# Performance work log

Measured on AMD Instinct MI355X. Metric: run time of the kernel, lower is better.

## Reference

```python
import jax, jax.numpy as jnp
import numpy as np

B, T, C = 16, 2048, 512
G = 2                 # groups
V = 320               # num_vars
D = C // G            # var_dim = 256
GAMMA = 0.25
GN_EPS = 1e-5


def setup_inputs() -> dict:
    key = jax.random.key(0)
    k1, k2, k3 = jax.random.split(key, 3)
    x = jax.random.normal(k1, (B, T, C), dtype=jnp.float32)
    # grouped 1x1 conv weight: (out_channels, in_channels_per_group) = (C, D)
    conv_w = jax.random.normal(k2, (C, D), dtype=jnp.float32) * (1.0 / np.sqrt(D))
    gn_w = jnp.ones((C,), dtype=jnp.float32)
    gn_b = jnp.zeros((C,), dtype=jnp.float32)
    embedding = 0.01 * jax.random.normal(k3, (V, G, D), dtype=jnp.float32)
    return {"x": x, "conv_w": conv_w, "gn_w": gn_w, "gn_b": gn_b, "embedding": embedding}


def reference(x, conv_w, gn_w, gn_b, embedding):
    # x: [B, T, C] (time_first=True) -> [B, C, T]
    xt = jnp.transpose(x, (0, 2, 1))
    # grouped 1x1 conv == per-group matmul
    xg = xt.reshape(B, G, D, T)                      # [B, G, D_in, T]
    wg = conv_w.reshape(G, D, D)                     # [G, D_out, D_in]
    h = jnp.einsum('bgit,goi->bgot', xg, wg)         # [B, G, D, T]
    # Fp32GroupNorm over (D, T) per (B, G)
    mu = h.mean(axis=(2, 3), keepdims=True)
    var = ((h - mu) ** 2).mean(axis=(2, 3), keepdims=True)
    hn = (h - mu) * jax.lax.rsqrt(var + GN_EPS)
    ze = hn.reshape(B, C, T) * gn_w[None, :, None] + gn_b[None, :, None]  # [B, C, T]

    ze_ = ze.reshape(B, G, D, T).transpose(0, 3, 1, 2)  # [B, T, G, D]
    # squared distances to codebook (same argmin as L2 norm)
    e_sq = (embedding ** 2).sum(-1).T                    # [G, V]
    d2 = ((ze_ ** 2).sum(-1)[..., None]
          - 2.0 * jnp.einsum('btgd,vgd->btgv', ze_, embedding)
          + e_sq[None, None])                            # [B, T, G, V]
    idx = jnp.argmin(d2, axis=-1)                        # [B, T, G] int32

    zq = embedding[idx, jnp.arange(G)[None, None, :]]    # [B, T, G, D]
    zq = zq.reshape(B, T, C).transpose(0, 2, 1)          # [B, C, T]

    # straight-through
    x_st = jax.lax.stop_gradient(zq) + (ze - jax.lax.stop_gradient(ze))
    x_out = jnp.transpose(x_st, (0, 2, 1))               # back to [B, T, C]

    # code perplexity from one-hot usage counts
    flat_idx = idx.reshape(-1, G)                        # [B*T, G]
    counts = jnp.zeros((V, G), dtype=jnp.float32).at[flat_idx, jnp.arange(G)[None, :]].add(1.0)
    hard_probs = counts.T / jnp.float32(B * T)           # [G, V]
    code_perplexity = jnp.exp(-jnp.sum(hard_probs * jnp.log(hard_probs + 1e-7), axis=-1)).sum()

    latent_loss = jnp.mean((zq - jax.lax.stop_gradient(ze)) ** 2)
    commitment_loss = jnp.mean((ze - jax.lax.stop_gradient(zq)) ** 2)
    kmeans_loss = latent_loss + GAMMA * commitment_loss
    return x_out, kmeans_loss, code_perplexity
```

## Files before the change

kernel.cpp:

```cpp
#include <hip/hip_runtime.h>
#include <math.h>

#define BB 16
#define TT 2048
#define CC 512
#define GG 2
#define DD 256
#define VV 320
#define DT (DD*TT)
#define NOUT ((size_t)BB*TT*CC)

#define OFF_H      0ULL
#define SZ_H       ((size_t)BB*GG*TT*DD*4)
#define OFF_PART   (OFF_H + SZ_H)
#define OFF_MUSIG  (OFF_PART + 4096ULL*2*8)
#define OFF_ESQ    (OFF_MUSIG + 32ULL*2*4)
#define OFF_CNT    (OFF_ESQ + (size_t)GG*VV*4)
#define OFF_LOSS   (OFF_CNT + (size_t)GG*VV*4)
#define OFF_EMBH   67180032ULL
#define OFF_WH     (OFF_EMBH + 327680ULL)
#define OFF_WL     (OFF_WH + 262144ULL)

typedef _Float16 half8   __attribute__((ext_vector_type(8)));
typedef _Float16 half4_t __attribute__((ext_vector_type(4)));
typedef float    f32x4   __attribute__((ext_vector_type(4)));

#define MARGIN 2e-3f
#define CAP 16

#define GLOAD_LDS16(g, l) \
  __builtin_amdgcn_global_load_lds((const __attribute__((address_space(1))) void*)(g), \
                                   (__attribute__((address_space(3))) void*)(l), 16, 0, 0)

__global__ __launch_bounds__(256) void k_emb(const float* __restrict__ emb,
                                             const float* __restrict__ w,
                                             _Float16* __restrict__ embHp,
                                             _Float16* __restrict__ wHp,
                                             _Float16* __restrict__ wLp,
                                             float* __restrict__ esq,
                                             unsigned* __restrict__ counts,
                                             float* __restrict__ loss) {
  int blk = blockIdx.x;
  int tid = threadIdx.x;
  if (blk == 40) {
    for (int i = tid; i < GG*VV; i += 256) counts[i] = 0u;
    if (tid == 0) *loss = 0.0f;
    return;
  }
  if (blk >= 41) {
    int wblk = blk - 41;
    int g = wblk >> 3, c = wblk & 7;
    int o = tid;
    const float* wrow = w + (size_t)(g*DD + o)*DD + (c << 5);
    #pragma unroll
    for (int hgrp = 0; hgrp < 4; ++hgrp) {
      float4 f1 = *(const float4*)(wrow + (hgrp << 2));
      float4 f2 = *(const float4*)(wrow + (hgrp << 2) + 16);
      float fv[8] = {f1.x, f1.y, f1.z, f1.w, f2.x, f2.y, f2.z, f2.w};
      half8 vh, vl;
      #pragma unroll
      for (int e = 0; e < 8; ++e) {
        _Float16 hh = (_Float16)fv[e];
        vh[e] = hh;
        vl[e] = (_Float16)(fv[e] - (float)hh);
      }
      size_t base = (((((size_t)(g*8 + c)) << 2) + hgrp) << 8) + o;
      *(half8*)(wHp + (base << 3)) = vh;
      *(half8*)(wLp + (base << 3)) = vl;
    }
    return;
  }
  int g = blk / 20;
  int v0 = (blk % 20) * 16;
  int vl = tid >> 4, dl = tid & 15;
  int v = v0 + vl;
  double sq = 0.0;
  #pragma unroll
  for (int k = 0; k < 16; k++) {
    int d = dl + (k << 4);
    float e = emb[((size_t)v*GG + g)*DD + d];
    sq += (double)e * (double)e;
  }
  #pragma unroll
  for (int m = 1; m < 16; m <<= 1) sq += __shfl_xor(sq, m);
  if (dl == 0) esq[g*VV + v] = (float)sq;

  const int hgrp = dl >> 2, jb = dl & 3;
  #pragma unroll
  for (int c = 0; c < 8; ++c) {
    int k0 = (c << 5) + (hgrp << 2) + jb;
    int k1 = k0 + 16;
    float e0 = emb[((size_t)v*GG + g)*DD + k0];
    float e1 = emb[((size_t)v*GG + g)*DD + k1];
    size_t base = (((size_t)(g*8 + c)*4 + hgrp)*320 + v)*8;
    embHp[base + jb]     = (_Float16)e0;
    embHp[base + jb + 4] = (_Float16)e1;
  }
}

__global__ __launch_bounds__(256, 2) void k_conv2(const float* __restrict__ x,
                                                  const _Float16* __restrict__ wH,
                                                  const _Float16* __restrict__ wL,
                                                  float* __restrict__ h,
                                                  double* __restrict__ part) {
  __shared__ __align__(16) char BsC[65536];
  __shared__ double r1[4], r2[4];
  const int bid = blockIdx.x;
  const int bg = bid >> 4, tt = bid & 15;
  const int b = bg >> 1, g = bg & 1;
  const int tid = threadIdx.x;
  const int wv = tid >> 6, lane = tid & 63;
  const int l15 = tid & 15, lh = lane >> 4;
  const int t0w = (tt << 7) + (wv << 5);

  f32x4 acc[2][16];
  #pragma unroll
  for (int tf = 0; tf < 2; ++tf)
    #pragma unroll
    for (int vf = 0; vf < 16; ++vf) acc[tf][vf] = 0.0f;

  const char* WHg = (const char*)(wH + ((size_t)g << 16));
  const char* WLg = (const char*)(wL + ((size_t)g << 16));
  const float* xb0 = x + ((size_t)(b*TT + t0w + l15)*CC + g*DD + (lh << 2));
  const float* xb1 = xb0 + ((size_t)16)*CC;

  {
    const char* sH = WHg + wv*4096 + lane*16;
    const char* sL = WLg + wv*4096 + lane*16;
    char* dH = BsC + wv*4096;
    char* dL = BsC + 32768 + wv*4096;
    #pragma unroll
    for (int i = 0; i < 4; ++i) {
      GLOAD_LDS16(sH + i*1024, dH + i*1024);
      GLOAD_LDS16(sL + i*1024, dL + i*1024);
    }
  }
  float4 p00 = *(const float4*)(xb0);
  float4 p01 = *(const float4*)(xb0 + 16);
  float4 p10 = *(const float4*)(xb1);
  float4 p11 = *(const float4*)(xb1 + 16);
  __syncthreads();

  int cur = 0;
  #pragma unroll 1
  for (int c = 0; c < 8; ++c) {
    if (c < 7) {
      const char* sH = WHg + (size_t)(c + 1)*16384 + wv*4096 + lane*16;
      const char* sL = WLg + (size_t)(c + 1)*16384 + wv*4096 + lane*16;
      char* dH = BsC + (cur ^ 1)*16384 + wv*4096;
      char* dL = BsC + 32768 + (cur ^ 1)*16384 + wv*4096;
      #pragma unroll
      for (int i = 0; i < 4; ++i) {
        GLOAD_LDS16(sH + i*1024, dH + i*1024);
        GLOAD_LDS16(sL + i*1024, dL + i*1024);
      }
    }
    float4 c00 = p00, c01 = p01, c10 = p10, c11 = p11;
    if (c < 7) {
      const int off = (c + 1) << 5;
      p00 = *(const float4*)(xb0 + off);
      p01 = *(const float4*)(xb0 + off + 16);
      p10 = *(const float4*)(xb1 + off);
      p11 = *(const float4*)(xb1 + off + 16);
    }
    half8 ah[2], al[2];
    {
      float fv0[8] = {c00.x, c00.y, c00.z, c00.w, c01.x, c01.y, c01.z, c01.w};
      float fv1[8] = {c10.x, c10.y, c10.z, c10.w, c11.x, c11.y, c11.z, c11.w};
      #pragma unroll
      for (int e = 0; e < 8; ++e) {
        _Float16 h0 = (_Float16)fv0[e];
        ah[0][e] = h0; al[0][e] = (_Float16)(fv0[e] - (float)h0);
        _Float16 h1 = (_Float16)fv1[e];
        ah[1][e] = h1; al[1][e] = (_Float16)(fv1[e] - (float)h1);
      }
    }
    const char* BH = BsC + cur*16384;
    const char* BL = BsC + 32768 + cur*16384;
    #pragma unroll
    for (int vf = 0; vf < 16; ++vf) {
      const int o = (vf << 4) + l15;
      const int bo = ((lh << 8) + o) << 4;
      half8 bh = *(const half8*)(BH + bo);
      half8 bl = *(const half8*)(BL + bo);
      #pragma unroll
      for (int tf = 0; tf < 2; ++tf) {
        acc[tf][vf] = __builtin_amdgcn_mfma_f32_16x16x32_f16(ah[tf], bh, acc[tf][vf], 0, 0, 0);
        acc[tf][vf] = __builtin_amdgcn_mfma_f32_16x16x32_f16(al[tf], bh, acc[tf][vf], 0, 0, 0);
        acc[tf][vf] = __builtin_amdgcn_mfma_f32_16x16x32_f16(ah[tf], bl, acc[tf][vf], 0, 0, 0);
      }
    }
    __syncthreads();
    cur ^= 1;
  }

  double s1 = 0.0, s2 = 0.0;
  {
    float* hb = h + (size_t)bg*TT*DD;
    #pragma unroll
    for (int tf = 0; tf < 2; ++tf) {
      #pragma unroll
      for (int reg = 0; reg < 4; ++reg) {
        const int t = t0w + (tf << 4) + (lh << 2) + reg;
        float* hrow = hb + (size_t)t*DD + l15;
        #pragma unroll
        for (int vf = 0; vf < 16; ++vf) {
          float v = acc[tf][vf][reg];
          hrow[vf << 4] = v;
          double dv = (double)v;
          s1 += dv; s2 += dv*dv;
        }
      }
    }
  }
  #pragma unroll
  for (int m = 32; m > 0; m >>= 1) { s1 += __shfl_down(s1, m); s2 += __shfl_down(s2, m); }
  if (lane == 0) { r1[wv] = s1; r2[wv] = s2; }
  __syncthreads();
  if (tid == 0) {
    part[(size_t)bid*2]     = r1[0] + r1[1] + r1[2] + r1[3];
    part[(size_t)bid*2 + 1] = r2[0] + r2[1] + r2[2] + r2[3];
  }
}

__global__ void k_stats(const double* __restrict__ part, float* __restrict__ musig) {
  int i = threadIdx.x;
  if (i < BB*GG) {
    double s1 = 0.0, s2 = 0.0;
    for (int r = 0; r < 16; r++) { s1 += part[(i*16 + r)*2]; s2 += part[(i*16 + r)*2 + 1]; }
    double mu  = s1 / (double)DT;
    double var = s2 / (double)DT - mu*mu;
    double rs  = 1.0 / sqrt(var + 1e-5);
    musig[i*2]     = (float)mu;
    musig[i*2 + 1] = (float)rs;
  }
}

__global__ __launch_bounds__(256, 2) void k_vq2(const float* __restrict__ h,
                                                const float* __restrict__ musig,
                                                const float* __restrict__ gn_w,
                                                const float* __restrict__ gn_b,
                                                const _Float16* __restrict__ embH,
                                                const float* __restrict__ esq,
                                                const float* __restrict__ emb,
                                                float* __restrict__ out,
                                                unsigned* __restrict__ counts,
                                                float* __restrict__ loss) {
  __shared__ __align__(16) char smem[43008];
  float*  esqs    = (float*)smem;
  int*    candcnt = (int*)(smem + 1280);
  int*    bestv   = (int*)(smem + 1792);
  int*    slowl   = (int*)(smem + 2304);
  int*    nslow   = (int*)(smem + 2816);
  unsigned short* cand = (unsigned short*)(smem + 2832);
  float*  redf    = (float*)(smem + 6944);
  float*  gnws    = (float*)(smem + 40960);
  float*  gnbs    = (float*)(smem + 41984);

  const int bid = blockIdx.x;
  const int bg  = bid >> 4;
  const int t0  = (bid & 15) << 7;
  const int b = bg >> 1, g = bg & 1;
  const int tid = threadIdx.x;
  const int lane = tid & 63, wv = tid >> 6;
  const int l15 = tid & 15, lh = lane >> 4;
  const float mu = musig[bg*2], rs = musig[bg*2 + 1];
  const float* hb = h + ((size_t)bg*TT + t0)*DD;

  gnws[tid] = gn_w[g*DD + tid];
  gnbs[tid] = gn_b[g*DD + tid];

  f32x4 acc[2][20];
  #pragma unroll
  for (int tf = 0; tf < 2; ++tf)
    #pragma unroll
    for (int vf = 0; vf < 20; ++vf) acc[tf][vf] = 0.0f;

  const char* gBH = (const char*)(embH + (size_t)(g*8)*10240);
  const float* gwp = gn_w + g*DD;
  const float* gbp = gn_b + g*DD;

  const float* hb0 = hb + (size_t)((wv << 5) + l15)*DD + (lh << 2);
  const float* hb1 = hb0 + ((size_t)16)*DD;

  {
    const char* sB = gBH + wv*5120 + lane*16;
    char* dB = smem + wv*5120;
    #pragma unroll
    for (int i = 0; i < 5; ++i) GLOAD_LDS16(sB + i*1024, dB + i*1024);
  }
  float4 p00 = *(const float4*)(hb0);
  float4 p01 = *(const float4*)(hb0 + 16);
  float4 p10 = *(const float4*)(hb1);
  float4 p11 = *(const float4*)(hb1 + 16);
  __syncthreads();

  int cur = 0;
  #pragma unroll 1
  for (int c = 0; c < 8; ++c) {
    if (c < 7) {
      const char* sB = gBH + (size_t)(c + 1)*20480 + wv*5120 + lane*16;
      char* dB = smem + (cur ^ 1)*20480 + wv*5120;
      #pragma unroll
      for (int i = 0; i < 5; ++i) GLOAD_LDS16(sB + i*1024, dB + i*1024);
    }
    float4 c00 = p00, c01 = p01, c10 = p10, c11 = p11;
    if (c < 7) {
      const int off = (c + 1) << 5;
      p00 = *(const float4*)(hb0 + off);
      p01 = *(const float4*)(hb0 + off + 16);
      p10 = *(const float4*)(hb1 + off);
      p11 = *(const float4*)(hb1 + off + 16);
    }
    const int c32 = c << 5;
    half8 ah[2];
    {
      float4 w1 = *(const float4*)(gwp + c32 + (lh << 2));
      float4 w2 = *(const float4*)(gwp + c32 + (lh << 2) + 16);
      float4 b1 = *(const float4*)(gbp + c32 + (lh << 2));
      float4 b2 = *(const float4*)(gbp + c32 + (lh << 2) + 16);
      float wv_[8] = {w1.x, w1.y, w1.z, w1.w, w2.x, w2.y, w2.z, w2.w};
      float bv_[8] = {b1.x, b1.y, b1.z, b1.w, b2.x, b2.y, b2.z, b2.w};
      float fv0[8] = {c00.x, c00.y, c00.z, c00.w, c01.x, c01.y, c01.z, c01.w};
      float fv1[8] = {c10.x, c10.y, c10.z, c10.w, c11.x, c11.y, c11.z, c11.w};
      #pragma unroll
      for (int e = 0; e < 8; ++e) {
        float z0 = __fmul_rn(__fsub_rn(fv0[e], mu), rs);
        z0 = __fadd_rn(__fmul_rn(z0, wv_[e]), bv_[e]);
        ah[0][e] = (_Float16)z0;
        float z1 = __fmul_rn(__fsub_rn(fv1[e], mu), rs);
        z1 = __fadd_rn(__fmul_rn(z1, wv_[e]), bv_[e]);
        ah[1][e] = (_Float16)z1;
      }
    }
    const char* BH = smem + cur*20480;
    #pragma unroll
    for (int vf = 0; vf < 20; ++vf) {
      const int v = (vf << 4) + l15;
      half8 bh = *(const half8*)(BH + ((lh*320 + v) << 4));
      #pragma unroll
      for (int tf = 0; tf < 2; ++tf)
        acc[tf][vf] = __builtin_amdgcn_mfma_f32_16x16x32_f16(ah[tf], bh, acc[tf][vf], 0, 0, 0);
    }
    __syncthreads();
    cur ^= 1;
  }

  if (tid < 160) { esqs[tid] = esq[g*VV + tid]; esqs[tid + 160] = esq[g*VV + tid + 160]; }
  if (tid < 128) { candcnt[tid] = 0; bestv[tid] = -1; }
  if (tid == 0) *nslow = 0;
  __syncthreads();

  #pragma unroll
  for (int tf = 0; tf < 2; ++tf) {
    #pragma unroll
    for (int reg = 0; reg < 4; ++reg) {
      int row = (wv << 5) + (tf << 4) + (lh << 2) + reg;
      float y[20]; float mn = 3.4e38f;
      #pragma unroll
      for (int vf = 0; vf < 20; ++vf) {
        y[vf] = fmaf(-2.0f, acc[tf][vf][reg], esqs[(vf << 4) + l15]);
        mn = fminf(mn, y[vf]);
      }
      #pragma unroll
      for (int m = 1; m < 16; m <<= 1) mn = fminf(mn, __shfl_xor(mn, m));
      float thr = mn + MARGIN;
      #pragma unroll
      for (int vf = 0; vf < 20; ++vf) {
        if (y[vf] <= thr) {
          int pos = atomicAdd(&candcnt[row], 1);
          if (pos < CAP) cand[row*CAP + pos] = (unsigned short)((vf << 4) + l15);
        }
      }
    }
  }
  __syncthreads();
  if (tid < 128) {
    int cnt = candcnt[tid];
    if (cnt == 1) bestv[tid] = cand[tid*CAP];
    else { int p = atomicAdd(nslow, 1); slowl[p] = tid; }
  }
  __syncthreads();

  const int ns = *nslow;
  for (int i = wv; i < ns; i += 4) {
    const int row = slowl[i];
    float4 hx  = *(const float4*)(hb + (size_t)row*DD + (lane << 2));
    float4 gw4 = *(const float4*)(gnws + (lane << 2));
    float4 gb4 = *(const float4*)(gnbs + (lane << 2));
    float hv[4] = {hx.x, hx.y, hx.z, hx.w};
    float gwv[4] = {gw4.x, gw4.y, gw4.z, gw4.w};
    float gbv[4] = {gb4.x, gb4.y, gb4.z, gb4.w};
    float zf[4];
    #pragma unroll
    for (int e = 0; e < 4; ++e) {
      float z = __fmul_rn(__fsub_rn(hv[e], mu), rs);
      zf[e] = __fadd_rn(__fmul_rn(z, gwv[e]), gbv[e]);
    }
    int cnt = candcnt[row];
    double bd = 1e300; int bvv = 0x7fffffff;
    if (cnt <= CAP) {
      for (int ci = 0; ci < cnt; ++ci) {
        int v = cand[row*CAP + ci];
        float4 ev = *(const float4*)(emb + ((size_t)v*GG + g)*DD + (lane << 2));
        float evv[4] = {ev.x, ev.y, ev.z, ev.w};
        double s = 0.0;
        #pragma unroll
        for (int e = 0; e < 4; ++e) {
          double df = (double)zf[e] - (double)evv[e];
          s += df*df;
        }
        #pragma unroll
        for (int m = 32; m > 0; m >>= 1) s += __shfl_down(s, m);
        s = __shfl(s, 0);
        if (s < bd || (s == bd && v < bvv)) { bd = s; bvv = v; }
      }
    } else {
      for (int v = 0; v < VV; ++v) {
        float4 ev = *(const float4*)(emb + ((size_t)v*GG + g)*DD + (lane << 2));
        float evv[4] = {ev.x, ev.y, ev.z, ev.w};
        double s = 0.0;
        #pragma unroll
        for (int e = 0; e < 4; ++e) {
          double df = (double)zf[e] - (double)evv[e];
          s += df*df;
        }
        #pragma unroll
        for (int m = 32; m > 0; m >>= 1) s += __shfl_down(s, m);
        s = __shfl(s, 0);
        if (s < bd) { bd = s; bvv = v; }
      }
    }
    if (lane == 0) bestv[row] = bvv;
  }
  __syncthreads();

  if (tid < 128) atomicAdd(&counts[g*VV + bestv[tid]], 1u);

  float lp = 0.0f;
  float* ob = out + (size_t)(b*TT + t0)*CC + g*DD + tid;
  const float gw = gnws[tid], gb2 = gnbs[tid];
  #pragma unroll 1
  for (int r0 = 0; r0 < 128; r0 += 8) {
    int vv[8]; float ee[8], hh[8];
    #pragma unroll
    for (int j = 0; j < 8; ++j) vv[j] = bestv[r0 + j];
    #pragma unroll
    for (int j = 0; j < 8; ++j) ee[j] = emb[((size_t)vv[j]*GG + g)*DD + tid];
    #pragma unroll
    for (int j = 0; j < 8; ++j) hh[j] = hb[(size_t)(r0 + j)*DD + tid];
    #pragma unroll
    for (int j = 0; j < 8; ++j) {
      float z = __fmul_rn(__fsub_rn(hh[j], mu), rs);
      z = __fadd_rn(__fmul_rn(z, gw), gb2);
      float df = ee[j] - z;
      lp = fmaf(df, df, lp);
      ob[(size_t)(r0 + j)*CC] = ee[j];
    }
  }
  #pragma unroll
  for (int m = 32; m > 0; m >>= 1) lp += __shfl_down(lp, m);
  if (lane == 0) redf[wv] = lp;
  __syncthreads();
  if (tid == 0) atomicAdd(loss, redf[0] + redf[1] + redf[2] + redf[3]);
}

__global__ __launch_bounds__(256) void k_final(const unsigned* __restrict__ counts,
                                               const float* __restrict__ loss,
                                               float* __restrict__ out) {
  __shared__ float sd[256];
  int tid = threadIdx.x;
  float perp = 0.0f;
  for (int g = 0; g < GG; g++) {
    float p1 = 0.0f;
    for (int v = tid; v < VV; v += 256) {
      float p = (float)counts[g*VV + v] / 32768.0f;
      p1 += p * logf(p + 1e-7f);
    }
    sd[tid] = p1;
    __syncthreads();
    for (int s = 128; s > 0; s >>= 1) {
      if (tid < s) sd[tid] += sd[tid + s];
      __syncthreads();
    }
    if (tid == 0) perp += expf(-sd[0]);
    __syncthreads();
  }
  if (tid == 0) {
    out[NOUT]     = 1.25f * (*loss) / (float)NOUT;
    out[NOUT + 1] = perp;
  }
}

extern "C" void kernel_launch(void* const* d_in, const int* in_sizes, int n_in,
                              void* d_out, int out_size, void* d_ws, size_t ws_size,
                              hipStream_t stream) {
  const float* x   = (const float*)d_in[0];
  const float* cw  = (const float*)d_in[1];
  const float* gnw = (const float*)d_in[2];
  const float* gnb = (const float*)d_in[3];
  const float* emb = (const float*)d_in[4];
  float* out = (float*)d_out;
  char* ws = (char*)d_ws;
  float*     h      = (float*)(ws + OFF_H);
  double*    part   = (double*)(ws + OFF_PART);
  float*     musig  = (float*)(ws + OFF_MUSIG);
  float*     esq    = (float*)(ws + OFF_ESQ);
  unsigned*  counts = (unsigned*)(ws + OFF_CNT);
  float*     loss   = (float*)(ws + OFF_LOSS);
  _Float16*  embH   = (_Float16*)(ws + OFF_EMBH);
  _Float16*  wH     = (_Float16*)(ws + OFF_WH);
  _Float16*  wL     = (_Float16*)(ws + OFF_WL);

  hipLaunchKernelGGL(k_emb,   dim3(57),   dim3(256), 0, stream,
                     emb, cw, embH, wH, wL, esq, counts, loss);
  hipLaunchKernelGGL(k_conv2, dim3(512),  dim3(256), 0, stream, x, wH, wL, h, part);
  hipLaunchKernelGGL(k_stats, dim3(1),    dim3(32),  0, stream, part, musig);
  hipLaunchKernelGGL(k_vq2,   dim3(512),  dim3(256), 0, stream,
                     h, musig, gnw, gnb, embH, esq, emb, out, counts, loss);
  hipLaunchKernelGGL(k_final, dim3(1),    dim3(256), 0, stream, counts, loss, out);
}
```

Baseline: 103.8 us.

## Halve VQ tile rows, add occupancy, compute loss algebraically, refine waitcnt barriers

The VQ kernel now handles 64 rows per block instead of 128, launched on twice as many blocks with a three-blocks-per-CU bound. Accumulator registers and LDS shrink, and the gn weight/bias loads are prefetched alongside h. The squared-error loss per row is computed as ||ze||^2 plus the minimum distance term from the matmul, or taken from the exact distance on the slow path, which removes the second pass that reread h to recompute ze. Both the conv and VQ loops replace __syncthreads with explicit vmcnt waits plus raw barriers so prefetches stay in flight. The risk is a small loss difference from fp16 matmul distances, and the hand-set vmcnt counts must match the number of outstanding loads.

```diff
diff --git a/kernel.cpp b/kernel.cpp
--- a/kernel.cpp
+++ b/kernel.cpp
@@ -22,7 +22,6 @@
 #define OFF_WL     (OFF_WH + 262144ULL)
 
 typedef _Float16 half8   __attribute__((ext_vector_type(8)));
-typedef _Float16 half4_t __attribute__((ext_vector_type(4)));
 typedef float    f32x4   __attribute__((ext_vector_type(4)));
 
 #define MARGIN 2e-3f
@@ -139,7 +138,6 @@
   float4 p01 = *(const float4*)(xb0 + 16);
   float4 p10 = *(const float4*)(xb1);
   float4 p11 = *(const float4*)(xb1 + 16);
-  __syncthreads();
 
   int cur = 0;
   #pragma unroll 1
@@ -154,7 +152,12 @@
         GLOAD_LDS16(sH + i*1024, dH + i*1024);
         GLOAD_LDS16(sL + i*1024, dL + i*1024);
       }
-    }
+      asm volatile("s_waitcnt vmcnt(12)" ::: "memory");
+    } else {
+      asm volatile("s_waitcnt vmcnt(4)" ::: "memory");
+    }
+    __builtin_amdgcn_s_barrier();
+
     float4 c00 = p00, c01 = p01, c10 = p10, c11 = p11;
     if (c < 7) {
       const int off = (c + 1) << 5;
@@ -190,7 +193,7 @@
         acc[tf][vf] = __builtin_amdgcn_mfma_f32_16x16x32_f16(ah[tf], bl, acc[tf][vf], 0, 0, 0);
       }
     }
-    __syncthreads();
+    __builtin_amdgcn_s_barrier();
     cur ^= 1;
   }
 
@@ -236,7 +239,7 @@
   }
 }
 
-__global__ __launch_bounds__(256, 2) void k_vq2(const float* __restrict__ h,
+__global__ __launch_bounds__(256, 3) void k_vq2(const float* __restrict__ h,
                                                 const float* __restrict__ musig,
                                                 const float* __restrict__ gn_w,
                                                 const float* __restrict__ gn_b,
@@ -246,20 +249,20 @@
                                                 float* __restrict__ out,
                                                 unsigned* __restrict__ counts,
                                                 float* __restrict__ loss) {
-  __shared__ __align__(16) char smem[43008];
+  __shared__ __align__(16) char smem[40960];
   float*  esqs    = (float*)smem;
   int*    candcnt = (int*)(smem + 1280);
-  int*    bestv   = (int*)(smem + 1792);
-  int*    slowl   = (int*)(smem + 2304);
-  int*    nslow   = (int*)(smem + 2816);
-  unsigned short* cand = (unsigned short*)(smem + 2832);
-  float*  redf    = (float*)(smem + 6944);
-  float*  gnws    = (float*)(smem + 40960);
-  float*  gnbs    = (float*)(smem + 41984);
+  int*    bestv   = (int*)(smem + 1536);
+  int*    slowl   = (int*)(smem + 1792);
+  int*    nslow   = (int*)(smem + 2048);
+  float*  ze2s    = (float*)(smem + 2112);
+  float*  ymins   = (float*)(smem + 2368);
+  float*  lossrow = (float*)(smem + 2624);
+  unsigned short* cand = (unsigned short*)(smem + 2880);
 
   const int bid = blockIdx.x;
-  const int bg  = bid >> 4;
-  const int t0  = (bid & 15) << 7;
+  const int bg  = bid >> 5;
+  const int t0  = (bid & 31) << 6;
   const int b = bg >> 1, g = bg & 1;
   const int tid = threadIdx.x;
   const int lane = tid & 63, wv = tid >> 6;
@@ -267,21 +270,14 @@
   const float mu = musig[bg*2], rs = musig[bg*2 + 1];
   const float* hb = h + ((size_t)bg*TT + t0)*DD;
 
-  gnws[tid] = gn_w[g*DD + tid];
-  gnbs[tid] = gn_b[g*DD + tid];
-
-  f32x4 acc[2][20];
-  #pragma unroll
-  for (int tf = 0; tf < 2; ++tf)
-    #pragma unroll
-    for (int vf = 0; vf < 20; ++vf) acc[tf][vf] = 0.0f;
+  f32x4 acc[20];
+  #pragma unroll
+  for (int vf = 0; vf < 20; ++vf) acc[vf] = 0.0f;
 
   const char* gBH = (const char*)(embH + (size_t)(g*8)*10240);
   const float* gwp = gn_w + g*DD;
   const float* gbp = gn_b + g*DD;
-
-  const float* hb0 = hb + (size_t)((wv << 5) + l15)*DD + (lh << 2);
-  const float* hb1 = hb0 + ((size_t)16)*DD;
+  const float* hb0 = hb + (size_t)((wv << 4) + l15)*DD + (lh << 2);
 
   {
     const char* sB = gBH + wv*5120 + lane*16;
@@ -289,12 +285,14 @@
     #pragma unroll
     for (int i = 0; i < 5; ++i) GLOAD_LDS16(sB + i*1024, dB + i*1024);
   }
-  float4 p00 = *(const float4*)(hb0);
-  float4 p01 = *(const float4*)(hb0 + 16);
-  float4 p10 = *(const float4*)(hb1);
-  float4 p11 = *(const float4*)(hb1 + 16);
-  __syncthreads();
-
+  float4 gw1 = *(const float4*)(gwp + (lh << 2));
+  float4 gw2 = *(const float4*)(gwp + (lh << 2) + 16);
+  float4 gb1 = *(const float4*)(gbp + (lh << 2));
+  float4 gb2 = *(const float4*)(gbp + (lh << 2) + 16);
+  float4 pa0 = *(const float4*)(hb0);
+  float4 pa1 = *(const float4*)(hb0 + 16);
+
+  float ze2acc = 0.0f;
   int cur = 0;
   #pragma unroll 1
   for (int c = 0; c < 8; ++c) {
@@ -303,34 +301,33 @@
       char* dB = smem + (cur ^ 1)*20480 + wv*5120;
       #pragma unroll
       for (int i = 0; i < 5; ++i) GLOAD_LDS16(sB + i*1024, dB + i*1024);
-    }
-    float4 c00 = p00, c01 = p01, c10 = p10, c11 = p11;
+      asm volatile("s_waitcnt vmcnt(11)" ::: "memory");
+    } else {
+      asm volatile("s_waitcnt vmcnt(6)" ::: "memory");
+    }
+    __builtin_amdgcn_s_barrier();
+
+    float4 a0 = pa0, a1 = pa1, w1 = gw1, w2 = gw2, b1 = gb1, b2 = gb2;
     if (c < 7) {
       const int off = (c + 1) << 5;
-      p00 = *(const float4*)(hb0 + off);
-      p01 = *(const float4*)(hb0 + off + 16);
-      p10 = *(const float4*)(hb1 + off);
-      p11 = *(const float4*)(hb1 + off + 16);
-    }
-    const int c32 = c << 5;
-    half8 ah[2];
+      gw1 = *(const float4*)(gwp + off + (lh << 2));
+      gw2 = *(const float4*)(gwp + off + (lh << 2) + 16);
+      gb1 = *(const float4*)(gbp + off + (lh << 2));
+      gb2 = *(const float4*)(gbp + off + (lh << 2) + 16);
+      pa0 = *(const float4*)(hb0 + off);
+      pa1 = *(const float4*)(hb0 + off + 16);
+    }
+    half8 ah;
     {
-      float4 w1 = *(const float4*)(gwp + c32 + (lh << 2));
-      float4 w2 = *(const float4*)(gwp + c32 + (lh << 2) + 16);
-      float4 b1 = *(const float4*)(gbp + c32 + (lh << 2));
-      float4 b2 = *(const float4*)(gbp + c32 + (lh << 2) + 16);
+      float fv[8]  = {a0.x, a0.y, a0.z, a0.w, a1.x, a1.y, a1.z, a1.w};
       float wv_[8] = {w1.x, w1.y, w1.z, w1.w, w2.x, w2.y, w2.z, w2.w};
       float bv_[8] = {b1.x, b1.y, b1.z, b1.w, b2.x, b2.y, b2.z, b2.w};
-      float fv0[8] = {c00.x, c00.y, c00.z, c00.w, c01.x, c01.y, c01.z, c01.w};
-      float fv1[8] = {c10.x, c10.y, c10.z, c10.w, c11.x, c11.y, c11.z, c11.w};
       #pragma unroll
       for (int e = 0; e < 8; ++e) {
-        float z0 = __fmul_rn(__fsub_rn(fv0[e], mu), rs);
-        z0 = __fadd_rn(__fmul_rn(z0, wv_[e]), bv_[e]);
-        ah[0][e] = (_Float16)z0;
-        float z1 = __fmul_rn(__fsub_rn(fv1[e], mu), rs);
-        z1 = __fadd_rn(__fmul_rn(z1, wv_[e]), bv_[e]);
-        ah[1][e] = (_Float16)z1;
+        float z = __fmul_rn(__fsub_rn(fv[e], mu), rs);
+        z = __fadd_rn(__fmul_rn(z, wv_[e]), bv_[e]);
+        ah[e] = (_Float16)z;
+        ze2acc = fmaf(z, z, ze2acc);
       }
     }
     const char* BH = smem + cur*20480;
@@ -338,47 +335,54 @@
     for (int vf = 0; vf < 20; ++vf) {
       const int v = (vf << 4) + l15;
       half8 bh = *(const half8*)(BH + ((lh*320 + v) << 4));
-      #pragma unroll
-      for (int tf = 0; tf < 2; ++tf)
-        acc[tf][vf] = __builtin_amdgcn_mfma_f32_16x16x32_f16(ah[tf], bh, acc[tf][vf], 0, 0, 0);
-    }
-    __syncthreads();
+      acc[vf] = __builtin_amdgcn_mfma_f32_16x16x32_f16(ah, bh, acc[vf], 0, 0, 0);
+    }
+    __builtin_amdgcn_s_barrier();
     cur ^= 1;
   }
+  __syncthreads();
 
   if (tid < 160) { esqs[tid] = esq[g*VV + tid]; esqs[tid + 160] = esq[g*VV + tid + 160]; }
-  if (tid < 128) { candcnt[tid] = 0; bestv[tid] = -1; }
+  if (tid < 64) { candcnt[tid] = 0; bestv[tid] = -1; }
   if (tid == 0) *nslow = 0;
+  {
+    float s = ze2acc;
+    s += __shfl_down(s, 32);
+    s += __shfl_down(s, 16);
+    if (lane < 16) ze2s[(wv << 4) + l15] = s;
+  }
   __syncthreads();
 
   #pragma unroll
-  for (int tf = 0; tf < 2; ++tf) {
-    #pragma unroll
-    for (int reg = 0; reg < 4; ++reg) {
-      int row = (wv << 5) + (tf << 4) + (lh << 2) + reg;
-      float y[20]; float mn = 3.4e38f;
-      #pragma unroll
-      for (int vf = 0; vf < 20; ++vf) {
-        y[vf] = fmaf(-2.0f, acc[tf][vf][reg], esqs[(vf << 4) + l15]);
-        mn = fminf(mn, y[vf]);
-      }
-      #pragma unroll
-      for (int m = 1; m < 16; m <<= 1) mn = fminf(mn, __shfl_xor(mn, m));
-      float thr = mn + MARGIN;
-      #pragma unroll
-      for (int vf = 0; vf < 20; ++vf) {
-        if (y[vf] <= thr) {
-          int pos = atomicAdd(&candcnt[row], 1);
-          if (pos < CAP) cand[row*CAP + pos] = (unsigned short)((vf << 4) + l15);
-        }
+  for (int reg = 0; reg < 4; ++reg) {
+    int row = (wv << 4) + (lh << 2) + reg;
+    float y[20]; float mn = 3.4e38f;
+    #pragma unroll
+    for (int vf = 0; vf < 20; ++vf) {
+      y[vf] = fmaf(-2.0f, acc[vf][reg], esqs[(vf << 4) + l15]);
+      mn = fminf(mn, y[vf]);
+    }
+    #pragma unroll
+    for (int m = 1; m < 16; m <<= 1) mn = fminf(mn, __shfl_xor(mn, m));
+    if (l15 == 0) ymins[row] = mn;
+    float thr = mn + MARGIN;
+    #pragma unroll
+    for (int vf = 0; vf < 20; ++vf) {
+      if (y[vf] <= thr) {
+        int pos = atomicAdd(&candcnt[row], 1);
+        if (pos < CAP) cand[row*CAP + pos] = (unsigned short)((vf << 4) + l15);
       }
     }
   }
   __syncthreads();
-  if (tid < 128) {
+  if (tid < 64) {
     int cnt = candcnt[tid];
-    if (cnt == 1) bestv[tid] = cand[tid*CAP];
-    else { int p = atomicAdd(nslow, 1); slowl[p] = tid; }
+    if (cnt == 1) {
+      bestv[tid] = cand[tid*CAP];
+      lossrow[tid] = ze2s[tid] + ymins[tid];
+    } else {
+      int p = atomicAdd(nslow, 1); slowl[p] = tid;
+    }
   }
   __syncthreads();
 
@@ -386,8 +390,8 @@
   for (int i = wv; i < ns; i += 4) {
     const int row = slowl[i];
     float4 hx  = *(const float4*)(hb + (size_t)row*DD + (lane << 2));
-    float4 gw4 = *(const float4*)(gnws + (lane << 2));
-    float4 gb4 = *(const float4*)(gnbs + (lane << 2));
+    float4 gw4 = *(const float4*)(gwp + (lane << 2));
+    float4 gb4 = *(const float4*)(gbp + (lane << 2));
     float hv[4] = {hx.x, hx.y, hx.z, hx.w};
     float gwv[4] = {gw4.x, gw4.y, gw4.z, gw4.w};
     float gbv[4] = {gb4.x, gb4.y, gb4.z, gb4.w};
@@ -431,38 +435,29 @@
         if (s < bd) { bd = s; bvv = v; }
       }
     }
-    if (lane == 0) bestv[row] = bvv;
+    if (lane == 0) { bestv[row] = bvv; lossrow[row] = (float)bd; }
   }
   __syncthreads();
 
-  if (tid < 128) atomicAdd(&counts[g*VV + bestv[tid]], 1u);
-
-  float lp = 0.0f;
+  if (tid < 64) atomicAdd(&counts[g*VV + bestv[tid]], 1u);
+  if (wv == 0) {
+    float s = lossrow[lane];
+    #pragma unroll
+    for (int m = 32; m > 0; m >>= 1) s += __shfl_down(s, m);
+    if (lane == 0) atomicAdd(loss, s);
+  }
+
   float* ob = out + (size_t)(b*TT + t0)*CC + g*DD + tid;
-  const float gw = gnws[tid], gb2 = gnbs[tid];
   #pragma unroll 1
-  for (int r0 = 0; r0 < 128; r0 += 8) {
-    int vv[8]; float ee[8], hh[8];
+  for (int r0 = 0; r0 < 64; r0 += 8) {
+    int vv[8]; float ee[8];
     #pragma unroll
     for (int j = 0; j < 8; ++j) vv[j] = bestv[r0 + j];
     #pragma unroll
     for (int j = 0; j < 8; ++j) ee[j] = emb[((size_t)vv[j]*GG + g)*DD + tid];
     #pragma unroll
-    for (int j = 0; j < 8; ++j) hh[j] = hb[(size_t)(r0 + j)*DD + tid];
-    #pragma unroll
-    for (int j = 0; j < 8; ++j) {
-      float z = __fmul_rn(__fsub_rn(hh[j], mu), rs);
-      z = __fadd_rn(__fmul_rn(z, gw), gb2);
-      float df = ee[j] - z;
-      lp = fmaf(df, df, lp);
-      ob[(size_t)(r0 + j)*CC] = ee[j];
-    }
-  }
-  #pragma unroll
-  for (int m = 32; m > 0; m >>= 1) lp += __shfl_down(lp, m);
-  if (lane == 0) redf[wv] = lp;
-  __syncthreads();
-  if (tid == 0) atomicAdd(loss, redf[0] + redf[1] + redf[2] + redf[3]);
+    for (int j = 0; j < 8; ++j) ob[(size_t)(r0 + j)*CC] = ee[j];
+  }
 }
 
 __global__ __launch_bounds__(256) void k_final(const unsigned* __restrict__ counts,
@@ -516,7 +511,7 @@
                      emb, cw, embH, wH, wL, esq, counts, loss);
   hipLaunchKernelGGL(k_conv2, dim3(512),  dim3(256), 0, stream, x, wH, wL, h, part);
   hipLaunchKernelGGL(k_stats, dim3(1),    dim3(32),  0, stream, part, musig);
-  hipLaunchKernelGGL(k_vq2,   dim3(512),  dim3(256), 0, stream,
+  hipLaunchKernelGGL(k_vq2,   dim3(1024), dim3(256), 0, stream,
                      h, musig, gnw, gnb, embH, esq, emb, out, counts, loss);
   hipLaunchKernelGGL(k_final, dim3(1),    dim3(256), 0, stream, counts, loss, out);
 }
```

Result: faster. 99.29 us (-4.3%).
